# Optimization experiments

Measured on AMD Instinct MI355X. Metric: run time of the kernel, lower is better.

Reference implementation:

```python
import jax, jax.numpy as jnp
import numpy as np

INPUT = 28
HID = 64
OUT = 10


def setup_inputs() -> dict:
    key = jax.random.key(0)
    ks = jax.random.split(key, 8)
    s_ih = 1.0 / np.sqrt(HID)
    x = jax.random.normal(ks[0], (16384, 28, INPUT), dtype=jnp.float32)
    # PyTorch LSTM params: gate order (i, f, g, o), each block of size HID
    W_ih = jax.random.uniform(ks[1], (4 * HID, INPUT), jnp.float32, -s_ih, s_ih)
    W_hh = jax.random.uniform(ks[2], (4 * HID, HID), jnp.float32, -s_ih, s_ih)
    b_ih = jax.random.uniform(ks[3], (4 * HID,), jnp.float32, -s_ih, s_ih)
    b_hh = jax.random.uniform(ks[4], (4 * HID,), jnp.float32, -s_ih, s_ih)
    s_fc = 1.0 / np.sqrt(HID)
    W_fc = jax.random.uniform(ks[5], (OUT, HID), jnp.float32, -s_fc, s_fc)
    b_fc = jax.random.uniform(ks[6], (OUT,), jnp.float32, -s_fc, s_fc)
    return {"x": x, "W_ih": W_ih, "W_hh": W_hh, "b_ih": b_ih, "b_hh": b_hh,
            "W_fc": W_fc, "b_fc": b_fc}


def reference(x, W_ih, W_hh, b_ih, b_hh, W_fc, b_fc):
    B = x.shape[0]
    # Precompute input projections for all timesteps in one big GEMM: [T, B, 4H]
    x_proj = jnp.einsum('bti,gi->tbg', x, W_ih) + (b_ih + b_hh)

    def step(carry, xp_t):
        h, c = carry
        gates = xp_t + h @ W_hh.T  # [B, 4H]
        i, f, g, o = jnp.split(gates, 4, axis=-1)
        i = jax.nn.sigmoid(i)
        f = jax.nn.sigmoid(f)
        g = jnp.tanh(g)
        o = jax.nn.sigmoid(o)
        c = f * c + i * g
        h = o * jnp.tanh(c)
        return (h, c), None

    h0 = jnp.zeros((B, HID), dtype=x.dtype)
    c0 = jnp.zeros((B, HID), dtype=x.dtype)
    (h_last, _), _ = jax.lax.scan(step, (h0, c0), x_proj)
    # fc on the last timestep's hidden state (== output[:, -1, :])
    return h_last @ W_fc.T + b_fc
```

## Files before the change

### kernel.cpp

```cpp
#include <hip/hip_runtime.h>
#include <hip/hip_bf16.h>


namespace {
constexpr int B_TOT   = 16384;
constexpr int T_STEPS = 28;
constexpr int IN_DIM  = 28;
constexpr int HID     = 64;
constexpr int OUT_DIM = 10;
constexpr int ROWS    = 16;
constexpr int THREADS = 256;
constexpr int KP      = 72;
constexpr int XROW    = T_STEPS * IN_DIM;
}

typedef __attribute__((ext_vector_type(8))) short short8v;
typedef __attribute__((ext_vector_type(4))) float float4v;
typedef __attribute__((ext_vector_type(4))) int   int4v;

__device__ __forceinline__ short f2bf_cold(float f) {
  union { float f; unsigned u; } v; v.f = f;
  unsigned r = v.u + 0x7FFFu + ((v.u >> 16) & 1u);
  return (short)(r >> 16);
}
__device__ __forceinline__ float bf2f(short s) {
  union { unsigned u; float f; } v; v.u = ((unsigned)(unsigned short)s) << 16;
  return v.f;
}
__device__ __forceinline__ unsigned pk2(float a, float b) {
  __hip_bfloat162 h = __float22bfloat162_rn(float2{a, b});
  union { __hip_bfloat162 h; unsigned u; } cv; cv.h = h; return cv.u;
}
__device__ __forceinline__ float sigf(float v) {
  return __builtin_amdgcn_rcpf(1.0f + __expf(-v));
}
__device__ __forceinline__ float tanh_f(float v) {
  return 2.0f * __builtin_amdgcn_rcpf(1.0f + __expf(-2.0f * v)) - 1.0f;
}

__global__ __attribute__((amdgpu_flat_work_group_size(THREADS, THREADS),
                          amdgpu_waves_per_eu(4, 4)))
void lstm_mfma4(const float* __restrict__ x, const float* __restrict__ W_ih,
                const float* __restrict__ W_hh, const float* __restrict__ b_ih,
                const float* __restrict__ b_hh, const float* __restrict__ W_fc,
                const float* __restrict__ b_fc, float* __restrict__ out) {
  __shared__ short hs[2][ROWS][KP];

  const int tid  = threadIdx.x;
  const int lane = tid & 63;
  const int w    = tid >> 6;
  const int l15  = lane & 15;
  const int q    = lane >> 4;
  const int b0   = blockIdx.x * ROWS;

  short8v a[4][3];
#pragma unroll
  for (int i = 0; i < 4; ++i) {
    const int mt   = 4 * w + i;
    const int m    = 16 * mt + l15;
    const int unit = m >> 2, type = m & 3;
    const int g    = type * 64 + unit;
#pragma unroll
    for (int kc = 0; kc < 3; ++kc) {
      short8v frag;
#pragma unroll
      for (int j = 0; j < 8; ++j) {
        const int k = kc * 32 + q * 8 + j;
        float v = 0.0f;
        if (k < IN_DIM)        v = W_ih[g * IN_DIM + k];
        else if (k == IN_DIM)  v = b_ih[g] + b_hh[g];
        else if (k >= 32)      v = W_hh[g * HID + (k - 32)];
        frag[j] = f2bf_cold(v);
      }
      a[i][kc] = frag;
    }
  }

  for (int idx = tid; idx < 2 * ROWS * KP; idx += THREADS) (&hs[0][0][0])[idx] = 0;
  __syncthreads();

  const float* xrow = x + (size_t)(b0 + l15) * XROW + q * 8;
  float4 lo = *(const float4*)xrow;
  float4 hi = {0.f, 0.f, 0.f, 0.f};
  if (q < 3) hi = *(const float4*)(xrow + 4);
  else       hi.x = 1.0f;

  float c_state[4] = {0.f, 0.f, 0.f, 0.f};

  for (int t = 0; t < T_STEPS; ++t) {
    const int cur = t & 1, nxt = cur ^ 1;

    int4v xi;
    xi[0] = pk2(lo.x, lo.y); xi[1] = pk2(lo.z, lo.w);
    xi[2] = pk2(hi.x, hi.y); xi[3] = pk2(hi.z, hi.w);
    union { int4v i; short8v s; } xb; xb.i = xi;

    short8v hf0 = *(const short8v*)&hs[cur][l15][q * 8];
    short8v hf1 = *(const short8v*)&hs[cur][l15][32 + q * 8];

    if (t + 1 < T_STEPS) {
      const float* xp = xrow + (t + 1) * IN_DIM;
      lo = *(const float4*)xp;
      if (q < 3) hi = *(const float4*)(xp + 4);
    }

    const float4v zero4 = {0.f, 0.f, 0.f, 0.f};
    float4v acc[4];
#pragma unroll
    for (int i = 0; i < 4; ++i)
      acc[i] = __builtin_amdgcn_mfma_f32_16x16x32_bf16(a[i][0], xb.s, zero4, 0, 0, 0);
#pragma unroll
    for (int i = 0; i < 4; ++i)
      acc[i] = __builtin_amdgcn_mfma_f32_16x16x32_bf16(a[i][1], hf0, acc[i], 0, 0, 0);
#pragma unroll
    for (int i = 0; i < 4; ++i)
      acc[i] = __builtin_amdgcn_mfma_f32_16x16x32_bf16(a[i][2], hf1, acc[i], 0, 0, 0);

    float hv[4];
#pragma unroll
    for (int i = 0; i < 4; ++i) {
      float4v g4 = acc[i];
      float iv = sigf(g4[0]);
      float fv = sigf(g4[1]);
      float gv = tanh_f(g4[2]);
      float ov = sigf(g4[3]);
      float cn = fv * c_state[i] + iv * gv;
      c_state[i] = cn;
      hv[i] = ov * tanh_f(cn);
    }
    unsigned p01 = pk2(hv[0], hv[1]);
    unsigned p23 = pk2(hv[2], hv[3]);
    hs[nxt][l15][16 * w + 0 + q]  = (short)(p01 & 0xFFFF);
    hs[nxt][l15][16 * w + 4 + q]  = (short)(p01 >> 16);
    hs[nxt][l15][16 * w + 8 + q]  = (short)(p23 & 0xFFFF);
    hs[nxt][l15][16 * w + 12 + q] = (short)(p23 >> 16);

    __syncthreads();
  }

  if (tid < ROWS * OUT_DIM) {
    const int r = tid / OUT_DIM;
    const int o = tid - r * OUT_DIM;
    float s = b_fc[o];
#pragma unroll
    for (int j = 0; j < HID; ++j)
      s += bf2f(hs[0][r][j]) * W_fc[o * HID + j];
    out[(b0 + r) * OUT_DIM + o] = s;
  }
}

extern "C" void kernel_launch(void* const* d_in, const int* in_sizes, int n_in,
                              void* d_out, int out_size, void* d_ws, size_t ws_size,
                              hipStream_t stream) {
  const float* x    = (const float*)d_in[0];
  const float* W_ih = (const float*)d_in[1];
  const float* W_hh = (const float*)d_in[2];
  const float* b_ih = (const float*)d_in[3];
  const float* b_hh = (const float*)d_in[4];
  const float* W_fc = (const float*)d_in[5];
  const float* b_fc = (const float*)d_in[6];
  float* out = (float*)d_out;

  dim3 grid(B_TOT / ROWS);
  dim3 block(THREADS);
  lstm_mfma4<<<grid, block, 0, stream>>>(x, W_ih, W_hh, b_ih, b_hh, W_fc, b_fc, out);
}
```

Before: 145.6 us.

## Stage x through LDS once per block and use Padé activations

Each block now loads its x rows into the shared h buffer using 112 stager threads and converts them to bf16 there. Previously all four waves loaded and packed the same x rows from global memory. The bias column is a constant 1.0 in LDS, h moves to columns 32..95, and all three MFMA B operands are read from LDS. Sigmoid and tanh are replaced by clamped rational Padé approximations with a single reciprocal, dropping the exp calls. The approximation error is small but nonzero for large-magnitude gate inputs.

Measured after the change: 157.8 us. 8.4% more time.

```diff
diff --git a/kernel.cpp b/kernel.cpp
--- a/kernel.cpp
+++ b/kernel.cpp
@@ -10,13 +10,13 @@
 constexpr int OUT_DIM = 10;
 constexpr int ROWS    = 16;
 constexpr int THREADS = 256;
-constexpr int KP      = 72;
+constexpr int KP      = 104;
 constexpr int XROW    = T_STEPS * IN_DIM;
 }
 
 typedef __attribute__((ext_vector_type(8))) short short8v;
+typedef __attribute__((ext_vector_type(4))) short short4v;
 typedef __attribute__((ext_vector_type(4))) float float4v;
-typedef __attribute__((ext_vector_type(4))) int   int4v;
 
 __device__ __forceinline__ short f2bf_cold(float f) {
   union { float f; unsigned u; } v; v.f = f;
@@ -31,16 +31,35 @@
   __hip_bfloat162 h = __float22bfloat162_rn(float2{a, b});
   union { __hip_bfloat162 h; unsigned u; } cv; cv.h = h; return cv.u;
 }
-__device__ __forceinline__ float sigf(float v) {
-  return __builtin_amdgcn_rcpf(1.0f + __expf(-v));
+
+__device__ __forceinline__ float tanh_pade(float x) {
+  float w = x * x;
+  float p = (w + 378.0f) * w + 17325.0f;
+  p = p * w + 135135.0f;
+  float num = x * p;
+  float q = 28.0f * w + 3150.0f;
+  q = q * w + 62370.0f;
+  q = q * w + 135135.0f;
+  float t = num * __builtin_amdgcn_rcpf(q);
+  return fminf(fmaxf(t, -1.0f), 1.0f);
 }
-__device__ __forceinline__ float tanh_f(float v) {
-  return 2.0f * __builtin_amdgcn_rcpf(1.0f + __expf(-2.0f * v)) - 1.0f;
+__device__ __forceinline__ float sig_pade(float v) {
+  float w = v * v;
+  float p = w * (1.0f / 128.0f) + 11.8125f;
+  p = p * w + 2165.625f;
+  p = p * w + 67567.5f;
+  float num = v * p;
+  float q = 0.4375f * w + 196.875f;
+  q = q * w + 15592.5f;
+  q = q * w + 135135.0f;
+  float t = num * __builtin_amdgcn_rcpf(q);
+  t = fminf(fmaxf(t, -1.0f), 1.0f);
+  return fmaf(t, 0.5f, 0.5f);
 }
 
 __global__ __attribute__((amdgpu_flat_work_group_size(THREADS, THREADS),
                           amdgpu_waves_per_eu(4, 4)))
-void lstm_mfma4(const float* __restrict__ x, const float* __restrict__ W_ih,
+void lstm_mfma5(const float* __restrict__ x, const float* __restrict__ W_ih,
                 const float* __restrict__ W_hh, const float* __restrict__ b_ih,
                 const float* __restrict__ b_hh, const float* __restrict__ W_fc,
                 const float* __restrict__ b_fc, float* __restrict__ out) {
@@ -78,62 +97,74 @@
 
   for (int idx = tid; idx < 2 * ROWS * KP; idx += THREADS) (&hs[0][0][0])[idx] = 0;
   __syncthreads();
+  if (tid < 2 * ROWS) hs[tid >> 4][tid & 15][IN_DIM] = (short)0x3F80;
 
-  const float* xrow = x + (size_t)(b0 + l15) * XROW + q * 8;
-  float4 lo = *(const float4*)xrow;
-  float4 hi = {0.f, 0.f, 0.f, 0.f};
-  if (q < 3) hi = *(const float4*)(xrow + 4);
-  else       hi.x = 1.0f;
+  const bool stager = (tid < ROWS * 7);
+  const int  sr = tid / 7;
+  const int  sc = tid - 7 * sr;
+  const float* xptr = x + (size_t)(b0 + sr) * XROW + sc * 4;
+
+  if (stager) {
+    float4 xv = *(const float4*)xptr;
+    short4v s;
+    unsigned plo = pk2(xv.x, xv.y), phi = pk2(xv.z, xv.w);
+    s[0] = (short)(plo & 0xFFFF); s[1] = (short)(plo >> 16);
+    s[2] = (short)(phi & 0xFFFF); s[3] = (short)(phi >> 16);
+    *(short4v*)&hs[0][sr][sc * 4] = s;
+  }
+  __syncthreads();
 
   float c_state[4] = {0.f, 0.f, 0.f, 0.f};
 
   for (int t = 0; t < T_STEPS; ++t) {
     const int cur = t & 1, nxt = cur ^ 1;
 
-    int4v xi;
-    xi[0] = pk2(lo.x, lo.y); xi[1] = pk2(lo.z, lo.w);
-    xi[2] = pk2(hi.x, hi.y); xi[3] = pk2(hi.z, hi.w);
-    union { int4v i; short8v s; } xb; xb.i = xi;
+    float4 xv;
+    const bool doStage = stager && (t + 1 < T_STEPS);
+    if (doStage) xv = *(const float4*)(xptr + (t + 1) * IN_DIM);
 
-    short8v hf0 = *(const short8v*)&hs[cur][l15][q * 8];
-    short8v hf1 = *(const short8v*)&hs[cur][l15][32 + q * 8];
-
-    if (t + 1 < T_STEPS) {
-      const float* xp = xrow + (t + 1) * IN_DIM;
-      lo = *(const float4*)xp;
-      if (q < 3) hi = *(const float4*)(xp + 4);
-    }
+    short8v bf0 = *(const short8v*)&hs[cur][l15][q * 8];
+    short8v bf1 = *(const short8v*)&hs[cur][l15][32 + q * 8];
+    short8v bf2 = *(const short8v*)&hs[cur][l15][64 + q * 8];
 
     const float4v zero4 = {0.f, 0.f, 0.f, 0.f};
     float4v acc[4];
 #pragma unroll
     for (int i = 0; i < 4; ++i)
-      acc[i] = __builtin_amdgcn_mfma_f32_16x16x32_bf16(a[i][0], xb.s, zero4, 0, 0, 0);
+      acc[i] = __builtin_amdgcn_mfma_f32_16x16x32_bf16(a[i][0], bf0, zero4, 0, 0, 0);
 #pragma unroll
     for (int i = 0; i < 4; ++i)
-      acc[i] = __builtin_amdgcn_mfma_f32_16x16x32_bf16(a[i][1], hf0, acc[i], 0, 0, 0);
+      acc[i] = __builtin_amdgcn_mfma_f32_16x16x32_bf16(a[i][1], bf1, acc[i], 0, 0, 0);
 #pragma unroll
     for (int i = 0; i < 4; ++i)
-      acc[i] = __builtin_amdgcn_mfma_f32_16x16x32_bf16(a[i][2], hf1, acc[i], 0, 0, 0);
+      acc[i] = __builtin_amdgcn_mfma_f32_16x16x32_bf16(a[i][2], bf2, acc[i], 0, 0, 0);
+
+    if (doStage) {
+      short4v s;
+      unsigned plo = pk2(xv.x, xv.y), phi = pk2(xv.z, xv.w);
+      s[0] = (short)(plo & 0xFFFF); s[1] = (short)(plo >> 16);
+      s[2] = (short)(phi & 0xFFFF); s[3] = (short)(phi >> 16);
+      *(short4v*)&hs[nxt][sr][sc * 4] = s;
+    }
 
     float hv[4];
 #pragma unroll
     for (int i = 0; i < 4; ++i) {
       float4v g4 = acc[i];
-      float iv = sigf(g4[0]);
-      float fv = sigf(g4[1]);
-      float gv = tanh_f(g4[2]);
-      float ov = sigf(g4[3]);
+      float iv = sig_pade(g4[0]);
+      float fv = sig_pade(g4[1]);
+      float gv = tanh_pade(g4[2]);
+      float ov = sig_pade(g4[3]);
       float cn = fv * c_state[i] + iv * gv;
       c_state[i] = cn;
-      hv[i] = ov * tanh_f(cn);
+      hv[i] = ov * tanh_pade(cn);
     }
     unsigned p01 = pk2(hv[0], hv[1]);
     unsigned p23 = pk2(hv[2], hv[3]);
-    hs[nxt][l15][16 * w + 0 + q]  = (short)(p01 & 0xFFFF);
-    hs[nxt][l15][16 * w + 4 + q]  = (short)(p01 >> 16);
-    hs[nxt][l15][16 * w + 8 + q]  = (short)(p23 & 0xFFFF);
-    hs[nxt][l15][16 * w + 12 + q] = (short)(p23 >> 16);
+    hs[nxt][l15][32 + 16 * w + 0 + q]  = (short)(p01 & 0xFFFF);
+    hs[nxt][l15][32 + 16 * w + 4 + q]  = (short)(p01 >> 16);
+    hs[nxt][l15][32 + 16 * w + 8 + q]  = (short)(p23 & 0xFFFF);
+    hs[nxt][l15][32 + 16 * w + 12 + q] = (short)(p23 >> 16);
 
     __syncthreads();
   }
@@ -144,7 +175,7 @@
     float s = b_fc[o];
 #pragma unroll
     for (int j = 0; j < HID; ++j)
-      s += bf2f(hs[0][r][j]) * W_fc[o * HID + j];
+      s += bf2f(hs[0][r][32 + j]) * W_fc[o * HID + j];
     out[(b0 + r) * OUT_DIM + o] = s;
   }
 }
@@ -163,5 +194,5 @@
 
   dim3 grid(B_TOT / ROWS);
   dim3 block(THREADS);
-  lstm_mfma4<<<grid, block, 0, stream>>>(x, W_ih, W_hh, b_ih, b_hh, W_fc, b_fc, out);
+  lstm_mfma5<<<grid, block, 0, stream>>>(x, W_ih, W_hh, b_ih, b_hh, W_fc, b_fc, out);
 }
```
